# Kernel optimization log

Measured on AMD Instinct MI355X. Metric: run time of the kernel, lower is better.

Reference implementation:

```python
import jax, jax.numpy as jnp
import numpy as np

B, N, H, E, OBS, A, AFF, EFF = 2, 50000, 64, 1_000_000, 128, 18, 512, 256


def setup_inputs() -> dict:
    key = jax.random.key(0)
    ks = jax.random.split(key, 20)
    s = 0.05  # small init to keep gates/tanh unsaturated
    return {
        "obs": jax.random.normal(ks[0], (B, OBS), jnp.float32),
        "state": jax.random.normal(ks[1], (B, N, H), jnp.float32) * 0.1,
        "W_in": jax.random.normal(ks[2], (OBS, H), jnp.float32) * s,
        "b_in": jnp.zeros((H,), jnp.float32),
        "W_msg": jax.random.normal(ks[3], (H, H), jnp.float32) * s,
        "W_gate": jax.random.normal(ks[4], (2 * H, H), jnp.float32) * s,
        "b_gate": jnp.zeros((H,), jnp.float32),
        "W_cand": jax.random.normal(ks[5], (2 * H, H), jnp.float32) * s,
        "b_cand": jnp.zeros((H,), jnp.float32),
        "W_dec": jax.random.normal(ks[6], (H, H), jnp.float32) * s,
        "b_dec": jnp.zeros((H,), jnp.float32),
        "W_mean": jax.random.normal(ks[7], (H, A), jnp.float32) * s,
        "b_mean": jnp.zeros((A,), jnp.float32),
        "W_ls": jax.random.normal(ks[8], (H, A), jnp.float32) * s,
        "b_ls": jnp.zeros((A,), jnp.float32),
        "src_index": jax.random.randint(ks[9], (E,), 0, N),
        "dst_index": jax.random.randint(ks[10], (E,), 0, N),
        "afferent_idx": jax.random.randint(ks[11], (AFF,), 0, N),
        "efferent_idx": jax.random.randint(ks[12], (EFF,), 0, N),
    }


def reference(obs, state, W_in, b_in, W_msg, W_gate, b_gate, W_cand, b_cand,
              W_dec, b_dec, W_mean, b_mean, W_ls, b_ls,
              src_index, dst_index, afferent_idx, efferent_idx):
    # inject obs projection into afferent node slots
    projected = obs @ W_in + b_in                                   # [B, H]
    injected = jnp.zeros_like(state).at[:, afferent_idx, :].set(projected[:, None, :])
    # gather-project-scatter message passing over the edge list
    src_msgs = state[:, src_index, :] @ W_msg                       # [B, E, H]
    messages = jnp.zeros_like(state).at[:, dst_index, :].add(src_msgs)
    # GRU-style gated update
    combined = messages + injected
    gate_in = jnp.concatenate([state, combined], axis=-1)           # [B, N, 2H]
    z = jax.nn.sigmoid(gate_in @ W_gate + b_gate)
    cand = jnp.tanh(gate_in @ W_cand + b_cand)
    next_state = (1.0 - z) * state + z * cand
    # mean-pool readout over efferent nodes, then policy heads
    readout = next_state[:, efferent_idx, :].mean(axis=1)           # [B, H]
    decoded = jnp.tanh(readout @ W_dec + b_dec)
    mean = decoded @ W_mean + b_mean
    log_std = jnp.clip(decoded @ W_ls + b_ls, -5.0, 2.0)
    return mean, log_std, next_state
```

## Files before the change

kernel.cpp:

```cpp
#include <hip/hip_runtime.h>
#include <hip/hip_bf16.h>

constexpr int kN   = 50000;
constexpr int kH   = 64;
constexpr int kB   = 2;
constexpr int kE   = 1000000;
constexpr int kObs = 128;
constexpr int kA   = 18;
constexpr int kAff = 512;
constexpr int kEff = 256;
constexpr int kNH  = kN * kH;
constexpr int kOutOff = 2 * kB * kA;
constexpr int kRanges = 8;
constexpr int kNr  = kN / kRanges;
constexpr int kChunks = 64;
constexpr int kEc  = kE / kChunks;
constexpr int kHistB = kRanges * kChunks;
constexpr int kPackBlocks = (kNH + 8191) / 8192;
constexpr int kWprepBlocks = 20;
constexpr int kScanB = (kN + 255) / 256;

typedef __attribute__((ext_vector_type(8))) short short8_t;
typedef __attribute__((ext_vector_type(4))) float f32x4_t;

__device__ __forceinline__ float ldf(const void* p, int i, int f32) {
  if (f32) return ((const float*)p)[i];
  unsigned short u = ((const unsigned short*)p)[i];
  union { unsigned int x; float f; } v; v.x = ((unsigned int)u) << 16; return v.f;
}
__device__ __forceinline__ void stf(void* p, int i, float val, int f32) {
  if (f32) ((float*)p)[i] = val;
  else ((__hip_bfloat16*)p)[i] = __float2bfloat16(val);
}
__device__ __forceinline__ float lo16(unsigned int w) {
  union { unsigned int i; float f; } v; v.i = w << 16; return v.f;
}
__device__ __forceinline__ float hi16(unsigned int w) {
  union { unsigned int i; float f; } v; v.i = w & 0xffff0000u; return v.f;
}
__device__ __forceinline__ float b2f(unsigned short u) {
  union { unsigned int i; float f; } v; v.i = ((unsigned int)u) << 16; return v.f;
}
__device__ __forceinline__ unsigned int f2b(float f) {
  union { float f; unsigned int u; } v; v.f = f;
  unsigned int r = v.u + 0x7fffu + ((v.u >> 16) & 1u);
  return r >> 16;
}
__device__ __forceinline__ float fsig(float x) {
  return __builtin_amdgcn_rcpf(1.f + __expf(-x));
}
__device__ __forceinline__ float ftanh(float x) {
  return 1.f - 2.f * __builtin_amdgcn_rcpf(__expf(2.f * x) + 1.f);
}
__device__ __forceinline__ int detect64(const unsigned short* wprobe, int t) {
  int hits = 0;
  for (int k = 0; k < 4; ++k) {
    unsigned short u = wprobe[(t * 4 + k) * 2];
    int e = (u >> 7) & 0xFF;
    if ((u & 0x7FFFu) != 0 && e >= 108 && e <= 128) hits++;
  }
  for (int off = 32; off; off >>= 1) hits += __shfl_down(hits, off);
  return (hits < 128) ? 1 : 0;
}

extern "C" __global__ __launch_bounds__(1024) void k_prep(
    const unsigned short* __restrict__ wprobe,
    const void* __restrict__ obs,
    const void* __restrict__ W_in,
    const void* __restrict__ b_in,
    const int* __restrict__ aff_idx,
    const int* __restrict__ dst,
    const void* __restrict__ W_msg,
    const void* __restrict__ W_gate,
    const void* __restrict__ W_cand,
    int* __restrict__ dflag,
    int* __restrict__ flags,
    float* __restrict__ projected,
    int* __restrict__ deg_c,
    unsigned short* __restrict__ wt) {
  __shared__ int sdeg[kNr];
  int t = threadIdx.x, b = blockIdx.x;
  if (b == 0) {
    __shared__ int sflag;
    if (t < 64) { int f = detect64(wprobe, t); if (t == 0) { sflag = f; dflag[0] = f; } }
    for (int i = t; i < kN; i += 1024) flags[i] = 0;
    __syncthreads();
    int f32 = sflag;
    if (t < kAff) flags[aff_idx[t]] = 1;
    if (t < kB * kH) {
      int bb = t >> 6, h = t & 63;
      float acc = ldf(b_in, h, f32);
      for (int o = 0; o < kObs; ++o)
        acc += ldf(obs, bb * kObs + o, f32) * ldf(W_in, o * kH + h, f32);
      projected[t] = acc;
    }
  } else if (b <= kHistB) {
    int h = b - 1, r = h & 7, c = h >> 3;
    int r0 = r * kNr;
    for (int i = t; i < kNr; i += 1024) sdeg[i] = 0;
    __syncthreads();
    int end = (c + 1) * kEc;
    for (int e = c * kEc + t; e < end; e += 1024) {
      unsigned rel = (unsigned)(dst[e] - r0);
      if (rel < (unsigned)kNr) atomicAdd(&sdeg[rel], 1);
    }
    __syncthreads();
    for (int i = t; i < kNr; i += 1024) deg_c[c * kN + r0 + i] = sdeg[i];
  } else {
    __shared__ int sflag;
    if (t < 64) { int f = detect64(wprobe, t); if (t == 0) sflag = f; }
    __syncthreads();
    int f32 = sflag;
    int i = (b - 1 - kHistB) * 1024 + t;
    if (i < 4096) {
      int n = i >> 6, k = i & 63;
      wt[i] = (unsigned short)f2b(ldf(W_msg, k * 64 + n, f32));
    } else if (i < 12288) {
      int j = i - 4096; int n = j >> 7, k = j & 127;
      wt[i] = (unsigned short)f2b(ldf(W_gate, k * 64 + n, f32));
    } else if (i < 20480) {
      int j = i - 12288; int n = j >> 7, k = j & 127;
      wt[i] = (unsigned short)f2b(ldf(W_cand, k * 64 + n, f32));
    }
  }
}

extern "C" __global__ void k_scan1(const int* __restrict__ deg_c,
                                   int* __restrict__ row_off,
                                   int* __restrict__ partials) {
  __shared__ int sd[256];
  int t = threadIdx.x;
  int n = blockIdx.x * 256 + t;
  int s = 0;
  if (n < kN) {
    for (int c = 0; c < kChunks; ++c) s += deg_c[c * kN + n];
  }
  sd[t] = s;
  __syncthreads();
  for (int off = 1; off < 256; off <<= 1) {
    int v = (t >= off) ? sd[t - off] : 0;
    __syncthreads();
    sd[t] += v;
    __syncthreads();
  }
  int excl = sd[t] - s;
  if (t == 255) partials[blockIdx.x] = sd[255];
  if (n < kN) row_off[n] = excl;
}

extern "C" __global__ void k_scan3(int* __restrict__ row_off,
                                   const int* __restrict__ partials,
                                   int* __restrict__ deg_c) {
  __shared__ int sd[256];
  int t = threadIdx.x;
  int s = 0;
  for (int j = t; j < (int)blockIdx.x; j += 256) s += partials[j];
  sd[t] = s;
  __syncthreads();
  for (int off = 128; off; off >>= 1) {
    if (t < off) sd[t] += sd[t + off];
    __syncthreads();
  }
  int base = sd[0];
  int n = blockIdx.x * 256 + t;
  if (n < kN) {
    int v = row_off[n] + base;
    row_off[n] = v;
    int run = v;
#pragma unroll 8
    for (int c = 0; c < kChunks; ++c) {
      int d = deg_c[c * kN + n];
      deg_c[c * kN + n] = run;
      run += d;
    }
  }
  if (blockIdx.x == 0 && t == 0) row_off[kN] = kE;
}

extern "C" __global__ __launch_bounds__(1024) void k_scatter(
    const int* __restrict__ src,
    const int* __restrict__ dst,
    const int* __restrict__ chunk_base,
    int* __restrict__ sorted_src,
    const unsigned short* __restrict__ wprobe,
    const void* __restrict__ state,
    unsigned int* __restrict__ pack) {
  __shared__ int scur[kNr];
  int t = threadIdx.x;
  if (blockIdx.x < kHistB) {
    int r = blockIdx.x & 7, c = blockIdx.x >> 3;
    int r0 = r * kNr;
    for (int i = t; i < kNr; i += 1024) scur[i] = chunk_base[c * kN + r0 + i];
    __syncthreads();
    int end = (c + 1) * kEc;
    for (int e = c * kEc + t; e < end; e += 1024) {
      unsigned rel = (unsigned)(dst[e] - r0);
      if (rel < (unsigned)kNr) {
        int pos = atomicAdd(&scur[rel], 1);
        sorted_src[pos] = src[e];
      }
    }
  } else {
    __shared__ int sflag;
    if (t < 64) { int f = detect64(wprobe, t); if (t == 0) sflag = f; }
    __syncthreads();
    int f32 = sflag;
    int i = (blockIdx.x - kHistB) * 8192 + t * 8;
    if (i < kNH) {
      uint4 o0, o1;
      if (!f32) {
        uint4 a = *(const uint4*)((const unsigned short*)state + i);
        uint4 c4 = *(const uint4*)((const unsigned short*)state + kNH + i);
        o0.x = (a.x & 0xffffu) | (c4.x << 16);
        o0.y = (a.x >> 16)     | (c4.x & 0xffff0000u);
        o0.z = (a.y & 0xffffu) | (c4.y << 16);
        o0.w = (a.y >> 16)     | (c4.y & 0xffff0000u);
        o1.x = (a.z & 0xffffu) | (c4.z << 16);
        o1.y = (a.z >> 16)     | (c4.z & 0xffff0000u);
        o1.z = (a.w & 0xffffu) | (c4.w << 16);
        o1.w = (a.w >> 16)     | (c4.w & 0xffff0000u);
      } else {
        const float* sf = (const float*)state;
        unsigned int w[8];
#pragma unroll
        for (int k = 0; k < 8; ++k)
          w[k] = f2b(sf[i + k]) | (f2b(sf[kNH + i + k]) << 16);
        o0 = make_uint4(w[0], w[1], w[2], w[3]);
        o1 = make_uint4(w[4], w[5], w[6], w[7]);
      }
      *(uint4*)&pack[i] = o0;
      *(uint4*)&pack[i + 4] = o1;
    }
  }
}

extern "C" __global__ __launch_bounds__(256) void k_update(
    const unsigned int* __restrict__ pk,
    const unsigned short* __restrict__ wt,
    const void* __restrict__ b_gate,
    const void* __restrict__ b_cand,
    const int* __restrict__ row_off,
    const int* __restrict__ sorted_src,
    const int* __restrict__ flags,
    const float* __restrict__ projected,
    const int* __restrict__ dflag,
    void* __restrict__ out) {
  __shared__ uint4 lx4[1088];
  unsigned short* lx = (unsigned short*)lx4;
  int f32 = dflag[0];
  int t = threadIdx.x;
  int w = t >> 6, lane = t & 63;
  int q = lane >> 4, l15 = lane & 15;
  int rowb = w * 16;
  int nd0 = blockIdx.x * 32;
  int ndw = nd0 + w * 8;

  const uint4* pk4 = (const uint4*)pk;
  for (int j = lane; j < 128; j += 64) {
    int ndl = j >> 4, c4 = j & 15;
    int ndg = min(ndw + ndl, kN - 1);
    uint4 pv = pk4[ndg * 16 + c4];
    int r0 = rowb + 2 * ndl;
    *(uint2*)&lx[r0 * 136 + c4 * 4] =
        make_uint2((pv.x & 0xffffu) | (pv.y << 16), (pv.z & 0xffffu) | (pv.w << 16));
    *(uint2*)&lx[(r0 + 1) * 136 + c4 * 4] =
        make_uint2((pv.x >> 16) | (pv.y & 0xffff0000u), (pv.z >> 16) | (pv.w & 0xffff0000u));
  }

  for (int ndl = 0; ndl < 8; ++ndl) {
    int n = ndw + ndl;
    if (n >= kN) break;
    int s = row_off[n], en = row_off[n + 1];
    float a0x = 0.f, a0y = 0.f, a0z = 0.f, a0w = 0.f;
    float a1x = 0.f, a1y = 0.f, a1z = 0.f, a1w = 0.f;
    for (int e = s; e < en; e += 8) {
#pragma unroll
      for (int h = 0; h < 2; ++h) {
        int ee = e + h * 4 + q;
        int idx = sorted_src[min(ee, en - 1)];
        uint4 wv = pk4[idx * 16 + l15];
        if (ee >= en) { wv.x = 0u; wv.y = 0u; wv.z = 0u; wv.w = 0u; }
        a0x += lo16(wv.x); a1x += hi16(wv.x);
        a0y += lo16(wv.y); a1y += hi16(wv.y);
        a0z += lo16(wv.z); a1z += hi16(wv.z);
        a0w += lo16(wv.w); a1w += hi16(wv.w);
      }
    }
    a0x += __shfl_xor(a0x, 16); a0x += __shfl_xor(a0x, 32);
    a0y += __shfl_xor(a0y, 16); a0y += __shfl_xor(a0y, 32);
    a0z += __shfl_xor(a0z, 16); a0z += __shfl_xor(a0z, 32);
    a0w += __shfl_xor(a0w, 16); a0w += __shfl_xor(a0w, 32);
    a1x += __shfl_xor(a1x, 16); a1x += __shfl_xor(a1x, 32);
    a1y += __shfl_xor(a1y, 16); a1y += __shfl_xor(a1y, 32);
    a1z += __shfl_xor(a1z, 16); a1z += __shfl_xor(a1z, 32);
    a1w += __shfl_xor(a1w, 16); a1w += __shfl_xor(a1w, 32);
    if (q == 0) {
      int r0 = rowb + 2 * ndl;
      *(uint2*)&lx[r0 * 136 + 64 + l15 * 4] =
          make_uint2(f2b(a0x) | (f2b(a0y) << 16), f2b(a0z) | (f2b(a0w) << 16));
      *(uint2*)&lx[(r0 + 1) * 136 + 64 + l15 * 4] =
          make_uint2(f2b(a1x) | (f2b(a1y) << 16), f2b(a1z) | (f2b(a1w) << 16));
    }
  }

  const unsigned short* wm = wt;
  const unsigned short* wg = wt + 4096;
  const unsigned short* wc = wt + 12288;

  short8_t a0 = *(const short8_t*)&lx[(rowb + l15) * 136 + 64 + q * 8];
  short8_t a1 = *(const short8_t*)&lx[(rowb + l15) * 136 + 96 + q * 8];
  f32x4_t msgc[4];
#pragma unroll
  for (int ct = 0; ct < 4; ++ct) {
    f32x4_t acc = {0.f, 0.f, 0.f, 0.f};
    short8_t b0 = *(const short8_t*)&wm[(ct * 16 + l15) * 64 + q * 8];
    short8_t b1 = *(const short8_t*)&wm[(ct * 16 + l15) * 64 + 32 + q * 8];
    acc = __builtin_amdgcn_mfma_f32_16x16x32_bf16(a0, b0, acc, 0, 0, 0);
    acc = __builtin_amdgcn_mfma_f32_16x16x32_bf16(a1, b1, acc, 0, 0, 0);
    msgc[ct] = acc;
  }
  int nA = nd0 + w * 8 + q * 2, nB = nA + 1;
  int flA = (nA < kN) ? flags[nA] : 0;
  int flB = (nB < kN) ? flags[nB] : 0;
#pragma unroll
  for (int ct = 0; ct < 4; ++ct) {
    int col = ct * 16 + l15;
    float pj0 = projected[col], pj1 = projected[64 + col];
#pragma unroll
    for (int r = 0; r < 4; ++r) {
      int row = rowb + q * 4 + r;
      int fl = (r < 2) ? flA : flB;
      float inj = fl ? ((row & 1) ? pj1 : pj0) : 0.f;
      lx[row * 136 + 64 + col] = (unsigned short)f2b(msgc[ct][r] + inj);
    }
  }

  short8_t xa[4];
#pragma unroll
  for (int ks = 0; ks < 4; ++ks)
    xa[ks] = *(const short8_t*)&lx[(rowb + l15) * 136 + ks * 32 + q * 8];
  float ps[16];
#pragma unroll
  for (int ct = 0; ct < 4; ++ct)
#pragma unroll
    for (int rp = 0; rp < 2; ++rp) {
      int row = rowb + q * 4 + 2 * rp;
      ps[ct * 4 + rp * 2 + 0] = b2f(lx[row * 136 + ct * 16 + l15]);
      ps[ct * 4 + rp * 2 + 1] = b2f(lx[(row + 1) * 136 + ct * 16 + l15]);
    }
  float* soutw = (float*)((char*)lx4 + w * 4352);
#pragma unroll
  for (int ct = 0; ct < 4; ++ct) {
    f32x4_t accg = {0.f, 0.f, 0.f, 0.f}, accc = {0.f, 0.f, 0.f, 0.f};
#pragma unroll
    for (int ks = 0; ks < 4; ++ks) {
      short8_t bg = *(const short8_t*)&wg[(ct * 16 + l15) * 128 + ks * 32 + q * 8];
      short8_t bc = *(const short8_t*)&wc[(ct * 16 + l15) * 128 + ks * 32 + q * 8];
      accg = __builtin_amdgcn_mfma_f32_16x16x32_bf16(xa[ks], bg, accg, 0, 0, 0);
      accc = __builtin_amdgcn_mfma_f32_16x16x32_bf16(xa[ks], bc, accc, 0, 0, 0);
    }
    int col = ct * 16 + l15;
    float bgv = ldf(b_gate, col, f32), bcv = ldf(b_cand, col, f32);
#pragma unroll
    for (int rp = 0; rp < 2; ++rp) {
      int r = q * 4 + 2 * rp;
      float z0 = fsig(accg[2 * rp] + bgv);
      float c0 = ftanh(accc[2 * rp] + bcv);
      soutw[r * 64 + col] = (1.f - z0) * ps[ct * 4 + rp * 2 + 0] + z0 * c0;
      float z1 = fsig(accg[2 * rp + 1] + bgv);
      float c1 = ftanh(accc[2 * rp + 1] + bcv);
      soutw[(r + 1) * 64 + col] = (1.f - z1) * ps[ct * 4 + rp * 2 + 1] + z1 * c1;
    }
  }
  __syncthreads();

  int nvalid = min(32, kN - nd0) * 64;
  if (f32) {
    float* po = (float*)out + kOutOff;
#pragma unroll
    for (int p = 0; p < 2; ++p)
      for (int j = t * 4; j < nvalid; j += 1024) {
        int ndl = j >> 6, c = j & 63;
        int wv = ndl >> 3, r = ((ndl & 7) << 1) + p;
        float4 v = *(float4*)((char*)lx4 + wv * 4352 + r * 256 + c * 4);
        *(float4*)(po + p * kNH + nd0 * 64 + j) = v;
      }
  } else {
    unsigned short* po = (unsigned short*)out + kOutOff;
#pragma unroll
    for (int p = 0; p < 2; ++p)
      for (int j = t * 8; j < nvalid; j += 2048) {
        int ndl = j >> 6, c = j & 63;
        int wv = ndl >> 3, r = ((ndl & 7) << 1) + p;
        const char* base = (const char*)lx4 + wv * 4352 + r * 256 + c * 4;
        float4 v0 = *(const float4*)base;
        float4 v1 = *(const float4*)(base + 16);
        uint4 o;
        o.x = f2b(v0.x) | (f2b(v0.y) << 16);
        o.y = f2b(v0.z) | (f2b(v0.w) << 16);
        o.z = f2b(v1.x) | (f2b(v1.y) << 16);
        o.w = f2b(v1.z) | (f2b(v1.w) << 16);
        *(uint4*)(po + p * kNH + nd0 * 64 + j) = o;
      }
  }
}

extern "C" __global__ void k_readout(const void* __restrict__ W_dec,
                                     const void* __restrict__ b_dec,
                                     const void* __restrict__ W_mean,
                                     const void* __restrict__ b_mean,
                                     const void* __restrict__ W_ls,
                                     const void* __restrict__ b_ls,
                                     const int* __restrict__ eff_idx,
                                     const int* __restrict__ dflag,
                                     void* __restrict__ out) {
  __shared__ float part[8][64];
  __shared__ float ro[128], dec[128];
  int f32 = dflag[0];
  int t = threadIdx.x;
  int wv = t >> 6, lane = t & 63;
  int b = wv >> 2, g = wv & 3;
  float acc = 0.f;
#pragma unroll 4
  for (int i = 0; i < 64; ++i) {
    int n = eff_idx[g * 64 + i];
    acc += ldf(out, kOutOff + b * kNH + n * 64 + lane, f32);
  }
  part[wv][lane] = acc;
  __syncthreads();
  if (t < 128) {
    int bb = t >> 6, h = t & 63;
    float s = part[bb * 4 + 0][h] + part[bb * 4 + 1][h] +
              part[bb * 4 + 2][h] + part[bb * 4 + 3][h];
    ro[t] = s * (1.f / kEff);
  }
  __syncthreads();
  if (t < 128) {
    int bb = t >> 6, h = t & 63;
    float d = ldf(b_dec, h, f32);
    for (int k = 0; k < 64; ++k) d += ro[bb * 64 + k] * ldf(W_dec, k * 64 + h, f32);
    dec[t] = tanhf(d);
  }
  __syncthreads();
  if (t < kB * kA) {
    int bb = t / kA, a = t % kA;
    float m = ldf(b_mean, a, f32), l = ldf(b_ls, a, f32);
    for (int k = 0; k < 64; ++k) {
      float dv = dec[bb * 64 + k];
      m += dv * ldf(W_mean, k * kA + a, f32);
      l += dv * ldf(W_ls, k * kA + a, f32);
    }
    l = fminf(fmaxf(l, -5.f), 2.f);
    stf(out, t, m, f32);
    stf(out, kB * kA + t, l, f32);
  }
}

extern "C" void kernel_launch(void* const* d_in, const int* in_sizes, int n_in,
                              void* d_out, int out_size, void* d_ws, size_t ws_size,
                              hipStream_t stream) {
  (void)in_sizes; (void)n_in; (void)out_size; (void)ws_size;
  const void* obs    = d_in[0];
  const void* state  = d_in[1];
  const void* W_in   = d_in[2];
  const void* b_in   = d_in[3];
  const void* W_msg  = d_in[4];
  const void* W_gate = d_in[5];
  const void* b_gate = d_in[6];
  const void* W_cand = d_in[7];
  const void* b_cand = d_in[8];
  const void* W_dec  = d_in[9];
  const void* b_dec  = d_in[10];
  const void* W_mean = d_in[11];
  const void* b_mean = d_in[12];
  const void* W_ls   = d_in[13];
  const void* b_ls   = d_in[14];
  const int* src = (const int*)d_in[15];
  const int* dst = (const int*)d_in[16];
  const int* aff = (const int*)d_in[17];
  const int* eff = (const int*)d_in[18];

  int* wsp        = (int*)d_ws;
  int* flags      = wsp;
  int* deg_c      = flags + kN;
  int* row_off    = deg_c + kChunks * kN;
  int* partials   = row_off + (kN + 64);
  int* dflag      = partials + 512;
  float* projected = (float*)(dflag + 16);
  int* sorted_src  = (int*)(projected + 128);
  unsigned int* pk  = (unsigned int*)(sorted_src + kE);
  unsigned short* wt = (unsigned short*)(pk + kNH);

  k_prep<<<1 + kHistB + kWprepBlocks, 1024, 0, stream>>>(
      (const unsigned short*)W_cand, obs, W_in, b_in, aff, dst,
      W_msg, W_gate, W_cand, dflag, flags, projected, deg_c, wt);
  k_scan1<<<kScanB, 256, 0, stream>>>(deg_c, row_off, partials);
  k_scan3<<<kScanB, 256, 0, stream>>>(row_off, partials, deg_c);
  k_scatter<<<kHistB + kPackBlocks, 1024, 0, stream>>>(
      src, dst, deg_c, sorted_src, (const unsigned short*)W_cand, state, pk);
  k_update<<<(kN + 31) / 32, 256, 0, stream>>>(pk, wt, b_gate, b_cand,
                                               row_off, sorted_src, flags,
                                               projected, dflag, d_out);
  k_readout<<<1, 512, 0, stream>>>(W_dec, b_dec, W_mean, b_mean, W_ls, b_ls, eff,
                                   dflag, d_out);
}
```

Measured before the change: 281.1 us.

## Split edge gather-aggregation into a separate one-node-per-wave kernel

Moves the per-node neighbor aggregation out of the update kernel into a new kernel where each wave handles one node. Before, each wave walked eight nodes in sequence inside the MFMA update kernel. The change aims for more parallelism and latency hiding on the irregular gather, and the update kernel now just loads packed aggregates. In exchange it adds a kernel launch and an extra round trip of about 12.8MB of aggregate data through global memory.

```diff
diff --git a/kernel.cpp b/kernel.cpp
--- a/kernel.cpp
+++ b/kernel.cpp
@@ -234,13 +234,57 @@
   }
 }
 
+extern "C" __global__ __launch_bounds__(256) void k_gather(
+    const unsigned int* __restrict__ pack,
+    const int* __restrict__ row_off,
+    const int* __restrict__ sorted_src,
+    unsigned int* __restrict__ agg) {
+  int wave = threadIdx.x >> 6, lane = threadIdx.x & 63;
+  int n = blockIdx.x * 4 + wave;
+  if (n >= kN) return;
+  int s  = row_off[n];
+  int en = row_off[n + 1];
+  int g = lane >> 4, col = lane & 15;
+  const uint4* pk4 = (const uint4*)pack;
+  float a0x = 0.f, a0y = 0.f, a0z = 0.f, a0w = 0.f;
+  float a1x = 0.f, a1y = 0.f, a1z = 0.f, a1w = 0.f;
+  for (int e = s; e < en; e += 8) {
+#pragma unroll
+    for (int h = 0; h < 2; ++h) {
+      int ee = e + h * 4 + g;
+      int idx = sorted_src[min(ee, en - 1)];
+      uint4 wv = pk4[idx * 16 + col];
+      if (ee >= en) { wv.x = 0u; wv.y = 0u; wv.z = 0u; wv.w = 0u; }
+      a0x += lo16(wv.x); a1x += hi16(wv.x);
+      a0y += lo16(wv.y); a1y += hi16(wv.y);
+      a0z += lo16(wv.z); a1z += hi16(wv.z);
+      a0w += lo16(wv.w); a1w += hi16(wv.w);
+    }
+  }
+  a0x += __shfl_xor(a0x, 16); a0x += __shfl_xor(a0x, 32);
+  a0y += __shfl_xor(a0y, 16); a0y += __shfl_xor(a0y, 32);
+  a0z += __shfl_xor(a0z, 16); a0z += __shfl_xor(a0z, 32);
+  a0w += __shfl_xor(a0w, 16); a0w += __shfl_xor(a0w, 32);
+  a1x += __shfl_xor(a1x, 16); a1x += __shfl_xor(a1x, 32);
+  a1y += __shfl_xor(a1y, 16); a1y += __shfl_xor(a1y, 32);
+  a1z += __shfl_xor(a1z, 16); a1z += __shfl_xor(a1z, 32);
+  a1w += __shfl_xor(a1w, 16); a1w += __shfl_xor(a1w, 32);
+  if (g == 0) {
+    uint4 o;
+    o.x = f2b(a0x) | (f2b(a1x) << 16);
+    o.y = f2b(a0y) | (f2b(a1y) << 16);
+    o.z = f2b(a0z) | (f2b(a1z) << 16);
+    o.w = f2b(a0w) | (f2b(a1w) << 16);
+    ((uint4*)agg)[n * 16 + col] = o;
+  }
+}
+
 extern "C" __global__ __launch_bounds__(256) void k_update(
     const unsigned int* __restrict__ pk,
     const unsigned short* __restrict__ wt,
     const void* __restrict__ b_gate,
     const void* __restrict__ b_cand,
-    const int* __restrict__ row_off,
-    const int* __restrict__ sorted_src,
+    const unsigned int* __restrict__ agg,
     const int* __restrict__ flags,
     const float* __restrict__ projected,
     const int* __restrict__ dflag,
@@ -256,51 +300,21 @@
   int ndw = nd0 + w * 8;
 
   const uint4* pk4 = (const uint4*)pk;
+  const uint4* ag4 = (const uint4*)agg;
   for (int j = lane; j < 128; j += 64) {
     int ndl = j >> 4, c4 = j & 15;
     int ndg = min(ndw + ndl, kN - 1);
     uint4 pv = pk4[ndg * 16 + c4];
+    uint4 av = ag4[ndg * 16 + c4];
     int r0 = rowb + 2 * ndl;
     *(uint2*)&lx[r0 * 136 + c4 * 4] =
         make_uint2((pv.x & 0xffffu) | (pv.y << 16), (pv.z & 0xffffu) | (pv.w << 16));
     *(uint2*)&lx[(r0 + 1) * 136 + c4 * 4] =
         make_uint2((pv.x >> 16) | (pv.y & 0xffff0000u), (pv.z >> 16) | (pv.w & 0xffff0000u));
-  }
-
-  for (int ndl = 0; ndl < 8; ++ndl) {
-    int n = ndw + ndl;
-    if (n >= kN) break;
-    int s = row_off[n], en = row_off[n + 1];
-    float a0x = 0.f, a0y = 0.f, a0z = 0.f, a0w = 0.f;
-    float a1x = 0.f, a1y = 0.f, a1z = 0.f, a1w = 0.f;
-    for (int e = s; e < en; e += 8) {
-#pragma unroll
-      for (int h = 0; h < 2; ++h) {
-        int ee = e + h * 4 + q;
-        int idx = sorted_src[min(ee, en - 1)];
-        uint4 wv = pk4[idx * 16 + l15];
-        if (ee >= en) { wv.x = 0u; wv.y = 0u; wv.z = 0u; wv.w = 0u; }
-        a0x += lo16(wv.x); a1x += hi16(wv.x);
-        a0y += lo16(wv.y); a1y += hi16(wv.y);
-        a0z += lo16(wv.z); a1z += hi16(wv.z);
-        a0w += lo16(wv.w); a1w += hi16(wv.w);
-      }
-    }
-    a0x += __shfl_xor(a0x, 16); a0x += __shfl_xor(a0x, 32);
-    a0y += __shfl_xor(a0y, 16); a0y += __shfl_xor(a0y, 32);
-    a0z += __shfl_xor(a0z, 16); a0z += __shfl_xor(a0z, 32);
-    a0w += __shfl_xor(a0w, 16); a0w += __shfl_xor(a0w, 32);
-    a1x += __shfl_xor(a1x, 16); a1x += __shfl_xor(a1x, 32);
-    a1y += __shfl_xor(a1y, 16); a1y += __shfl_xor(a1y, 32);
-    a1z += __shfl_xor(a1z, 16); a1z += __shfl_xor(a1z, 32);
-    a1w += __shfl_xor(a1w, 16); a1w += __shfl_xor(a1w, 32);
-    if (q == 0) {
-      int r0 = rowb + 2 * ndl;
-      *(uint2*)&lx[r0 * 136 + 64 + l15 * 4] =
-          make_uint2(f2b(a0x) | (f2b(a0y) << 16), f2b(a0z) | (f2b(a0w) << 16));
-      *(uint2*)&lx[(r0 + 1) * 136 + 64 + l15 * 4] =
-          make_uint2(f2b(a1x) | (f2b(a1y) << 16), f2b(a1z) | (f2b(a1w) << 16));
-    }
+    *(uint2*)&lx[r0 * 136 + 64 + c4 * 4] =
+        make_uint2((av.x & 0xffffu) | (av.y << 16), (av.z & 0xffffu) | (av.w << 16));
+    *(uint2*)&lx[(r0 + 1) * 136 + 64 + c4 * 4] =
+        make_uint2((av.x >> 16) | (av.y & 0xffff0000u), (av.z >> 16) | (av.w & 0xffff0000u));
   }
 
   const unsigned short* wm = wt;
@@ -319,7 +333,7 @@
     acc = __builtin_amdgcn_mfma_f32_16x16x32_bf16(a1, b1, acc, 0, 0, 0);
     msgc[ct] = acc;
   }
-  int nA = nd0 + w * 8 + q * 2, nB = nA + 1;
+  int nA = ndw + q * 2, nB = nA + 1;
   int flA = (nA < kN) ? flags[nA] : 0;
   int flB = (nB < kN) ? flags[nB] : 0;
 #pragma unroll
@@ -489,7 +503,8 @@
   float* projected = (float*)(dflag + 16);
   int* sorted_src  = (int*)(projected + 128);
   unsigned int* pk  = (unsigned int*)(sorted_src + kE);
-  unsigned short* wt = (unsigned short*)(pk + kNH);
+  unsigned int* agg = pk + kNH;
+  unsigned short* wt = (unsigned short*)(agg + kNH);
 
   k_prep<<<1 + kHistB + kWprepBlocks, 1024, 0, stream>>>(
       (const unsigned short*)W_cand, obs, W_in, b_in, aff, dst,
@@ -498,9 +513,9 @@
   k_scan3<<<kScanB, 256, 0, stream>>>(row_off, partials, deg_c);
   k_scatter<<<kHistB + kPackBlocks, 1024, 0, stream>>>(
       src, dst, deg_c, sorted_src, (const unsigned short*)W_cand, state, pk);
+  k_gather<<<(kN + 3) / 4, 256, 0, stream>>>(pk, row_off, sorted_src, agg);
   k_update<<<(kN + 31) / 32, 256, 0, stream>>>(pk, wt, b_gate, b_cand,
-                                               row_off, sorted_src, flags,
-                                               projected, dflag, d_out);
+                                               agg, flags, projected, dflag, d_out);
   k_readout<<<1, 512, 0, stream>>>(W_dec, b_dec, W_mean, b_mean, W_ls, b_ls, eff,
                                    dflag, d_out);
 }
```

Result: no change. 285.1 us (+1.4%).
